# Kernel tuning notes

Measured on AMD Instinct MI355X. Metric: run time of the kernel, lower is better.

## Reference

```python
import jax, jax.numpy as jnp
import numpy as np

N = 8192
IN_F = 512
OUT_F = 128


def setup_inputs() -> dict:
    key = jax.random.key(0)
    k1, k2, k3, k4, k5, k6 = jax.random.split(key, 6)
    inp = jax.random.normal(k1, (N, IN_F), dtype=jnp.float32)
    adj = jax.random.randint(k2, (N, N), 0, 2).astype(jnp.float32)
    M = jax.random.uniform(k3, (N, N), dtype=jnp.float32)
    W = jax.random.normal(k4, (IN_F, OUT_F), dtype=jnp.float32) * (1.414 * np.sqrt(2.0 / (IN_F + OUT_F)))
    a_self = jax.random.normal(k5, (OUT_F, 1), dtype=jnp.float32) * (1.414 * np.sqrt(2.0 / (OUT_F + 1)))
    a_neighs = jax.random.normal(k6, (OUT_F, 1), dtype=jnp.float32) * (1.414 * np.sqrt(2.0 / (OUT_F + 1)))
    return {"input": inp, "adj": adj, "M": M, "W": W, "a_self": a_self, "a_neighs": a_neighs}


def reference(input, adj, M, W, a_self, a_neighs):
    h = input @ W                       # [N, OUT_F]
    attn_self = h @ a_self              # [N, 1]
    attn_neighs = h @ a_neighs          # [N, 1]
    e = attn_self + attn_neighs.T       # [N, N] broadcast add
    e = jax.nn.leaky_relu(e * M, negative_slope=0.2)
    e = jnp.where(adj > 0, e, jnp.float32(-9e15))
    attention = jax.nn.softmax(e, axis=1)
    h_prime = attention @ h             # [N, OUT_F]
    return jax.nn.elu(h_prime)          # concat=True
```

## Files before the change

kernel.cpp:

```cpp
#include <hip/hip_runtime.h>
#include <hip/hip_bf16.h>

typedef __attribute__((ext_vector_type(4))) float f32x4;
typedef __attribute__((ext_vector_type(8))) short s16x8;

constexpr int NN   = 8192;
constexpr int KIN  = 512;
constexpr int KOUT = 128;

constexpr int JCHUNK = 4;
constexpr int JLEN   = NN / JCHUNK;
constexpr int SG     = 32;
constexpr int NS     = JLEN / SG;
constexpr int HBUF   = 8192;

__device__ __forceinline__ ushort f2bf(float x) {
    union { float f; unsigned u; } v; v.f = x;
    unsigned r = (v.u + 0x7fffu + ((v.u >> 16) & 1u)) >> 16;
    return (ushort)r;
}

__device__ __forceinline__ void gload_lds16(const void* g, void* l) {
    __builtin_amdgcn_global_load_lds((const __attribute__((address_space(1))) void*)g,
                                     (__attribute__((address_space(3))) void*)l, 16, 0, 0);
}

__global__ __launch_bounds__(256) void kA(const float* __restrict__ inp,
                                          const float* __restrict__ W,
                                          const float* __restrict__ a_s,
                                          const float* __restrict__ a_n,
                                          ushort* __restrict__ hT,
                                          float* __restrict__ s_out,
                                          float* __restrict__ t_out) {
    __shared__ float smem[16 * 512];
    const int t = threadIdx.x;
    const int rbase = blockIdx.x * 16;

#pragma unroll
    for (int it = 0; it < 8; ++it) {
        int idx = it * 256 + t;
        int r = idx >> 7;
        int c4 = (idx & 127) << 2;
        *(f32x4*)(&smem[r * 512 + c4]) =
            *(const f32x4*)(inp + (size_t)(rbase + r) * KIN + c4);
    }
    __syncthreads();

    const int c0 = (t & 31) * 4;
    const int rg = (t >> 5) * 2;
    float acc[2][4] = {};
#pragma unroll 4
    for (int k = 0; k < KIN; ++k) {
        f32x4 w4 = *(const f32x4*)(W + (size_t)k * KOUT + c0);
        float a0 = smem[(rg + 0) * 512 + k];
        float a1 = smem[(rg + 1) * 512 + k];
#pragma unroll
        for (int cc = 0; cc < 4; ++cc) {
            acc[0][cc] += a0 * w4[cc];
            acc[1][cc] += a1 * w4[cc];
        }
    }
    __syncthreads();

    float* h_lds = smem;
#pragma unroll
    for (int rr = 0; rr < 2; ++rr) {
        f32x4 v = {acc[rr][0], acc[rr][1], acc[rr][2], acc[rr][3]};
        *(f32x4*)(&h_lds[(rg + rr) * 128 + c0]) = v;
    }
    __syncthreads();

    {
        const int col = t >> 1;
        const int r0 = (t & 1) * 8;
        ushort tmp[8];
#pragma unroll
        for (int rr = 0; rr < 8; ++rr) tmp[rr] = f2bf(h_lds[(r0 + rr) * 128 + col]);
        *(f32x4*)(hT + (size_t)col * NN + rbase + r0) = *(f32x4*)&tmp[0];
    }

    {
        const int w = t >> 6, lane = t & 63;
        float as1 = a_s[lane], as2 = a_s[64 + lane];
        float an1 = a_n[lane], an2 = a_n[64 + lane];
#pragma unroll
        for (int rr = 0; rr < 4; ++rr) {
            int row = w * 4 + rr;
            float h1 = h_lds[row * 128 + lane];
            float h2 = h_lds[row * 128 + 64 + lane];
            float ps = h1 * as1 + h2 * as2;
            float pt = h1 * an1 + h2 * an2;
#pragma unroll
            for (int off = 32; off; off >>= 1) {
                ps += __shfl_xor(ps, off);
                pt += __shfl_xor(pt, off);
            }
            if (lane == 0) {
                s_out[rbase + row] = ps;
                t_out[rbase + row] = pt;
            }
        }
    }
}

__global__ __launch_bounds__(256, 2) void kB(const float* __restrict__ Mmat,
                                             const float* __restrict__ adjm,
                                             const ushort* __restrict__ hT,
                                             const float* __restrict__ s_in,
                                             const float* __restrict__ t_in,
                                             float* __restrict__ o_part,
                                             float* __restrict__ l_part) {
    __shared__ f32x4 LDSQ[3 * HBUF / 16];
    char* LDS = (char*)LDSQ;

    const int tid = threadIdx.x;
    const int w = tid >> 6;
    const int l = tid & 63;
    const int lrow = l & 15;
    const int kgrp = l >> 4;
    const int rb = blockIdx.x >> 2;
    const int jc = blockIdx.x & 3;
    const int j0 = jc * JLEN;
    const int i = rb * 64 + w * 16 + lrow;

    const float si = s_in[i];

    const float* Mp = Mmat + (size_t)i * NN + j0 + kgrp * 8;
    const float* Ap = adjm + (size_t)i * NN + j0 + kgrp * 8;
    const float* tp = t_in + j0 + kgrp * 8;

    const int rl8 = l >> 3;
    const int rl4 = l >> 2, c4i = l & 3;
    const int csH = c4i ^ (rl8 & 3);
    const ushort* gH0 = hT + (size_t)(w * 32 + rl4) * NN + j0 + csH * 8;
    const ushort* gH1 = gH0 + (size_t)16 * NN;
    const int hdst0 = (w * 32) * 64;
    const int hdst1 = (w * 32 + 16) * 64;
    const int Ch = lrow * 64 + ((kgrp ^ ((lrow >> 1) & 3)) << 4);

    f32x4 acc[8];
#pragma unroll
    for (int ct = 0; ct < 8; ++ct) acc[ct] = (f32x4){0.f, 0.f, 0.f, 0.f};
    float lsum = 0.f;

#define DMA_H(HB, SS)                                              \
    gload_lds16(gH0 + (size_t)(SS) * SG, LDS + (HB) + hdst0);      \
    gload_lds16(gH1 + (size_t)(SS) * SG, LDS + (HB) + hdst1);

#define LD_R(M0, M1, A0, A1, T0, T1, SS)                           \
    M0 = *(const f32x4*)(Mp + (SS) * SG);                          \
    M1 = *(const f32x4*)(Mp + (SS) * SG + 4);                      \
    A0 = *(const f32x4*)(Ap + (SS) * SG);                          \
    A1 = *(const f32x4*)(Ap + (SS) * SG + 4);                      \
    T0 = *(const f32x4*)(tp + (SS) * SG);                          \
    T1 = *(const f32x4*)(tp + (SS) * SG + 4);

#define COMPUTE(HB, M0, M1, A0, A1, T0, T1)                                      \
    {                                                                            \
        s16x8 af;                                                                \
        _Pragma("unroll")                                                        \
        for (int e = 0; e < 4; ++e) {                                            \
            float x = (si + (T0)[e]) * (M0)[e];                                  \
            x = fmaxf(x, 0.2f * x);                                              \
            float p = __expf(x) * (A0)[e];            \
            lsum += p;                                                           \
            af[e] = (short)f2bf(p);                                              \
        }                                                                        \
        _Pragma("unroll")                                                        \
        for (int e = 0; e < 4; ++e) {                                            \
            float x = (si + (T1)[e]) * (M1)[e];                                  \
            x = fmaxf(x, 0.2f * x);                                              \
            float p = __expf(x) * (A1)[e];                                       \
            lsum += p;                                                           \
            af[4 + e] = (short)f2bf(p);                                          \
        }                                                                        \
        const char* hb = LDS + (HB) + Ch;                                        \
        _Pragma("unroll")                                                        \
        for (int ct = 0; ct < 8; ++ct) {                                         \
            s16x8 bf = *(const s16x8*)(hb + ct * 1024);                          \
            acc[ct] = __builtin_amdgcn_mfma_f32_16x16x32_bf16(af, bf, acc[ct], 0, 0, 0); \
        }                                                                        \
    }

    f32x4 mA0, mA1, aA0, aA1, tA0, tA1;
    f32x4 mB0, mB1, aB0, aB1, tB0, tB1;
    int hA = 0, hB = HBUF, hC = 2 * HBUF;

    DMA_H(hA, 0)
    LD_R(mA0, mA1, aA0, aA1, tA0, tA1, 0)
    DMA_H(hB, 1)
    LD_R(mB0, mB1, aB0, aB1, tB0, tB1, 1)

#pragma unroll 1
    for (int s = 0; s < NS; s += 2) {
        const int s2 = (s + 2 < NS) ? s + 2 : NS - 1;
        const int s3 = (s + 3 < NS) ? s + 3 : NS - 1;

        asm volatile("s_waitcnt vmcnt(8)" ::: "memory");
        __builtin_amdgcn_s_barrier();
        asm volatile("" ::: "memory");
        DMA_H(hC, s2)
        COMPUTE(hA, mA0, mA1, aA0, aA1, tA0, tA1)
        LD_R(mA0, mA1, aA0, aA1, tA0, tA1, s2)

        asm volatile("s_waitcnt vmcnt(8)" ::: "memory");
        __builtin_amdgcn_s_barrier();
        asm volatile("" ::: "memory");
        DMA_H(hA, s3)
        COMPUTE(hB, mB0, mB1, aB0, aB1, tB0, tB1)
        LD_R(mB0, mB1, aB0, aB1, tB0, tB1, s3)

        int ht = hA; hA = hC; hC = hB; hB = ht;
    }
#undef DMA_H
#undef LD_R
#undef COMPUTE

    lsum += __shfl_xor(lsum, 16);
    lsum += __shfl_xor(lsum, 32);
    if (l < 16) l_part[(size_t)jc * NN + i] = lsum;

    float* op = o_part + (size_t)jc * NN * KOUT;
#pragma unroll
    for (int ct = 0; ct < 8; ++ct) {
#pragma unroll
        for (int r = 0; r < 4; ++r) {
            int gi = rb * 64 + w * 16 + kgrp * 4 + r;
            int col = ct * 16 + lrow;
            op[(size_t)gi * KOUT + col] = acc[ct][r];
        }
    }
}

__global__ __launch_bounds__(256) void kC(const float* __restrict__ o_part,
                                          const float* __restrict__ l_part,
                                          float* __restrict__ out) {
    const int idx = blockIdx.x * 256 + threadIdx.x;
    const int i = idx >> 7;
    float osum = 0.f, lsum = 0.f;
#pragma unroll
    for (int p = 0; p < JCHUNK; ++p) {
        osum += o_part[(size_t)p * NN * KOUT + idx];
        lsum += l_part[(size_t)p * NN + i];
    }
    float v = osum / lsum;
    out[idx] = v > 0.f ? v : (__expf(v) - 1.f);
}

extern "C" void kernel_launch(void* const* d_in, const int* in_sizes, int n_in,
                              void* d_out, int out_size, void* d_ws, size_t ws_size,
                              hipStream_t stream) {
    const float* inp = (const float*)d_in[0];
    const float* adj = (const float*)d_in[1];
    const float* Mm  = (const float*)d_in[2];
    const float* W   = (const float*)d_in[3];
    const float* a_s = (const float*)d_in[4];
    const float* a_n = (const float*)d_in[5];
    float* out = (float*)d_out;

    char* ws = (char*)d_ws;
    ushort* hT    = (ushort*)(ws + 0);
    float*  s_buf = (float*)(ws + 2097152);
    float*  t_buf = (float*)(ws + 2129920);
    float*  l_prt = (float*)(ws + 2162688);
    float*  o_prt = (float*)(ws + 4194304);

    hipLaunchKernelGGL(kA, dim3(512), dim3(256), 0, stream, inp, W, a_s, a_n, hT, s_buf, t_buf);
    hipLaunchKernelGGL(kB, dim3(128 * JCHUNK), dim3(256), 0, stream, Mm, adj, hT, s_buf, t_buf, o_prt, l_prt);
    hipLaunchKernelGGL(kC, dim3(4096), dim3(256), 0, stream, o_prt, l_prt, out);
}
```

Measured before the change: 203.5 us.

## Restructure attention kernel into 512-thread blocks with larger double-buffered h slabs

```diff
diff --git a/kernel.cpp b/kernel.cpp
--- a/kernel.cpp
+++ b/kernel.cpp
@@ -8,11 +8,12 @@
 constexpr int KIN  = 512;
 constexpr int KOUT = 128;
 
-constexpr int JCHUNK = 4;
-constexpr int JLEN   = NN / JCHUNK;
-constexpr int SG     = 32;
-constexpr int NS     = JLEN / SG;
-constexpr int HBUF   = 8192;
+constexpr int RBK  = 128;
+constexpr int JC   = 4;
+constexpr int JLEN = NN / JC;
+constexpr int SGO  = 128;
+constexpr int NS   = JLEN / SGO;
+constexpr int SLAB = 128 * 256;
 
 __device__ __forceinline__ ushort f2bf(float x) {
     union { float f; unsigned u; } v; v.f = x;
@@ -103,15 +104,14 @@
     }
 }
 
-__global__ __launch_bounds__(256, 2) void kB(const float* __restrict__ Mmat,
+__global__ __launch_bounds__(512, 2) void kG(const float* __restrict__ Mmat,
                                              const float* __restrict__ adjm,
                                              const ushort* __restrict__ hT,
                                              const float* __restrict__ s_in,
                                              const float* __restrict__ t_in,
                                              float* __restrict__ o_part,
                                              float* __restrict__ l_part) {
-    __shared__ f32x4 LDSQ[3 * HBUF / 16];
-    char* LDS = (char*)LDSQ;
+    __shared__ __align__(16) char slab[2][SLAB];
 
     const int tid = threadIdx.x;
     const int w = tid >> 6;
@@ -121,7 +121,9 @@
     const int rb = blockIdx.x >> 2;
     const int jc = blockIdx.x & 3;
     const int j0 = jc * JLEN;
-    const int i = rb * 64 + w * 16 + lrow;
+    const int row0 = rb * RBK;
+    const int i = row0 + w * 16 + lrow;
+    const int PH = rb & (NS - 1);
 
     const float si = s_in[i];
 
@@ -129,92 +131,93 @@
     const float* Ap = adjm + (size_t)i * NN + j0 + kgrp * 8;
     const float* tp = t_in + j0 + kgrp * 8;
 
-    const int rl8 = l >> 3;
-    const int rl4 = l >> 2, c4i = l & 3;
-    const int csH = c4i ^ (rl8 & 3);
-    const ushort* gH0 = hT + (size_t)(w * 32 + rl4) * NN + j0 + csH * 8;
-    const ushort* gH1 = gH0 + (size_t)16 * NN;
-    const int hdst0 = (w * 32) * 64;
-    const int hdst1 = (w * 32 + 16) * 64;
-    const int Ch = lrow * 64 + ((kgrp ^ ((lrow >> 1) & 3)) << 4);
+    const ushort* hq[4];
+#pragma unroll
+    for (int q = 0; q < 4; ++q) {
+        int r = w * 16 + q * 4 + (l >> 4);
+        int sc = ((l & 15) ^ (r & 7)) * 8;
+        hq[q] = hT + (size_t)r * NN + j0 + sc;
+    }
 
     f32x4 acc[8];
 #pragma unroll
     for (int ct = 0; ct < 8; ++ct) acc[ct] = (f32x4){0.f, 0.f, 0.f, 0.f};
     float lsum = 0.f;
 
-#define DMA_H(HB, SS)                                              \
-    gload_lds16(gH0 + (size_t)(SS) * SG, LDS + (HB) + hdst0);      \
-    gload_lds16(gH1 + (size_t)(SS) * SG, LDS + (HB) + hdst1);
-
-#define LD_R(M0, M1, A0, A1, T0, T1, SS)                           \
-    M0 = *(const f32x4*)(Mp + (SS) * SG);                          \
-    M1 = *(const f32x4*)(Mp + (SS) * SG + 4);                      \
-    A0 = *(const f32x4*)(Ap + (SS) * SG);                          \
-    A1 = *(const f32x4*)(Ap + (SS) * SG + 4);                      \
-    T0 = *(const f32x4*)(tp + (SS) * SG);                          \
-    T1 = *(const f32x4*)(tp + (SS) * SG + 4);
-
-#define COMPUTE(HB, M0, M1, A0, A1, T0, T1)                                      \
+    f32x4 gm0[4], gm1[4], ga0[4], ga1[4], gt0[4], gt1[4];
+
+#define DMA_HT(P, SL)                                                            \
+    _Pragma("unroll") for (int q = 0; q < 4; ++q)                                \
+        gload_lds16(hq[q] + (P) * SGO, &slab[SL][0] + (w * 16 + q * 4) * 256);
+
+#define LD_G(K, P)                                                               \
     {                                                                            \
+        const float* mp_ = Mp + (P) * SGO + (K) * 32;                            \
+        gm0[K] = *(const f32x4*)mp_;                                             \
+        gm1[K] = *(const f32x4*)(mp_ + 4);                                       \
+        const float* ap_ = Ap + (P) * SGO + (K) * 32;                            \
+        ga0[K] = *(const f32x4*)ap_;                                             \
+        ga1[K] = *(const f32x4*)(ap_ + 4);                                       \
+        const float* tp_ = tp + (P) * SGO + (K) * 32;                            \
+        gt0[K] = *(const f32x4*)tp_;                                             \
+        gt1[K] = *(const f32x4*)(tp_ + 4);                                       \
+    }
+
+#define KSTEP(K, SL, PN)                                                         \
+    {                                                                            \
+        asm volatile("s_waitcnt vmcnt(22)" ::: "memory");                        \
         s16x8 af;                                                                \
         _Pragma("unroll")                                                        \
         for (int e = 0; e < 4; ++e) {                                            \
-            float x = (si + (T0)[e]) * (M0)[e];                                  \
+            float x = (si + gt0[K][e]) * gm0[K][e];                              \
             x = fmaxf(x, 0.2f * x);                                              \
-            float p = __expf(x) * (A0)[e];            \
+            float p = __expf(x) * ga0[K][e];             \
             lsum += p;                                                           \
             af[e] = (short)f2bf(p);                                              \
         }                                                                        \
         _Pragma("unroll")                                                        \
         for (int e = 0; e < 4; ++e) {                                            \
-            float x = (si + (T1)[e]) * (M1)[e];                                  \
+            float x = (si + gt1[K][e]) * gm1[K][e];                              \
             x = fmaxf(x, 0.2f * x);                                              \
-            float p = __expf(x) * (A1)[e];                                       \
+            float p = __expf(x) * ga1[K][e];                                     \
             lsum += p;                                                           \
             af[4 + e] = (short)f2bf(p);                                          \
         }                                                                        \
-        const char* hb = LDS + (HB) + Ch;                                        \
+        const char* sb = &slab[SL][0];                                           \
         _Pragma("unroll")                                                        \
         for (int ct = 0; ct < 8; ++ct) {                                         \
-            s16x8 bf = *(const s16x8*)(hb + ct * 1024);                          \
+            s16x8 bf = *(const s16x8*)(sb + (ct * 16 + lrow) * 256 +             \
+                                       (((K) * 64 + kgrp * 16) ^ ((lrow & 7) << 4))); \
             acc[ct] = __builtin_amdgcn_mfma_f32_16x16x32_bf16(af, bf, acc[ct], 0, 0, 0); \
         }                                                                        \
-    }
-
-    f32x4 mA0, mA1, aA0, aA1, tA0, tA1;
-    f32x4 mB0, mB1, aB0, aB1, tB0, tB1;
-    int hA = 0, hB = HBUF, hC = 2 * HBUF;
-
-    DMA_H(hA, 0)
-    LD_R(mA0, mA1, aA0, aA1, tA0, tA1, 0)
-    DMA_H(hB, 1)
-    LD_R(mB0, mB1, aB0, aB1, tB0, tB1, 1)
+        LD_G(K, PN)                                                              \
+    }
+
+    DMA_HT(PH, 0)
+    LD_G(0, PH)
+    LD_G(1, PH)
+    LD_G(2, PH)
+    LD_G(3, PH)
+    asm volatile("s_waitcnt vmcnt(24)" ::: "memory");
+    __builtin_amdgcn_s_barrier();
+    asm volatile("" ::: "memory");
 
 #pragma unroll 1
-    for (int s = 0; s < NS; s += 2) {
-        const int s2 = (s + 2 < NS) ? s + 2 : NS - 1;
-        const int s3 = (s + 3 < NS) ? s + 3 : NS - 1;
-
-        asm volatile("s_waitcnt vmcnt(8)" ::: "memory");
+    for (int s = 0; s < NS; ++s) {
+        const int pn = (s + 1 + PH) & (NS - 1);
+        const int sl = s & 1;
+        DMA_HT(pn, (s + 1) & 1)
+        KSTEP(0, sl, pn)
+        KSTEP(1, sl, pn)
+        KSTEP(2, sl, pn)
+        KSTEP(3, sl, pn)
+        asm volatile("s_waitcnt vmcnt(24)" ::: "memory");
         __builtin_amdgcn_s_barrier();
         asm volatile("" ::: "memory");
-        DMA_H(hC, s2)
-        COMPUTE(hA, mA0, mA1, aA0, aA1, tA0, tA1)
-        LD_R(mA0, mA1, aA0, aA1, tA0, tA1, s2)
-
-        asm volatile("s_waitcnt vmcnt(8)" ::: "memory");
-        __builtin_amdgcn_s_barrier();
-        asm volatile("" ::: "memory");
-        DMA_H(hA, s3)
-        COMPUTE(hB, mB0, mB1, aB0, aB1, tB0, tB1)
-        LD_R(mB0, mB1, aB0, aB1, tB0, tB1, s3)
-
-        int ht = hA; hA = hC; hC = hB; hB = ht;
-    }
-#undef DMA_H
-#undef LD_R
-#undef COMPUTE
+    }
+#undef DMA_HT
+#undef LD_G
+#undef KSTEP
 
     lsum += __shfl_xor(lsum, 16);
     lsum += __shfl_xor(lsum, 32);
@@ -225,7 +228,7 @@
     for (int ct = 0; ct < 8; ++ct) {
 #pragma unroll
         for (int r = 0; r < 4; ++r) {
-            int gi = rb * 64 + w * 16 + kgrp * 4 + r;
+            int gi = row0 + w * 16 + kgrp * 4 + r;
             int col = ct * 16 + lrow;
             op[(size_t)gi * KOUT + col] = acc[ct][r];
         }
@@ -239,7 +242,7 @@
     const int i = idx >> 7;
     float osum = 0.f, lsum = 0.f;
 #pragma unroll
-    for (int p = 0; p < JCHUNK; ++p) {
+    for (int p = 0; p < JC; ++p) {
         osum += o_part[(size_t)p * NN * KOUT + idx];
         lsum += l_part[(size_t)p * NN + i];
     }
@@ -266,6 +269,6 @@
     float*  o_prt = (float*)(ws + 4194304);
 
     hipLaunchKernelGGL(kA, dim3(512), dim3(256), 0, stream, inp, W, a_s, a_n, hT, s_buf, t_buf);
-    hipLaunchKernelGGL(kB, dim3(128 * JCHUNK), dim3(256), 0, stream, Mm, adj, hT, s_buf, t_buf, o_prt, l_prt);
+    hipLaunchKernelGGL(kG, dim3(64 * JC), dim3(512), 0, stream, Mm, adj, hT, s_buf, t_buf, o_prt, l_prt);
     hipLaunchKernelGGL(kC, dim3(4096), dim3(256), 0, stream, o_prt, l_prt, out);
 }
```

New measurement: 177.6 us. 1.15x faster.
